# Performance work log

Hardware: AMD Instinct MI355X
Metric: run time of the kernel (lower is better)

The kernel has to match this reference:

```python
import jax, jax.numpy as jnp
import numpy as np

B, L, DIM, H, HD = 1, 2048, 3072, 24, 128
RANK, ALPHA, LORA_WEIGHT = 16, 16.0, 1.0
LORA_SCALE = ALPHA / RANK * LORA_WEIGHT


def _rope_pe(seq_len, head_dim, theta=10000.0):
    # Flux rope: pe[l, d/2, 2, 2] rotation matrices, returned as [1,1,L,d/2,2,2]
    pos = jnp.arange(seq_len, dtype=jnp.float32)
    omega = 1.0 / (theta ** (jnp.arange(0, head_dim, 2, dtype=jnp.float32) / head_dim))
    ang = pos[:, None] * omega[None, :]                      # [L, HD/2]
    cos, sin = jnp.cos(ang), jnp.sin(ang)
    pe = jnp.stack([jnp.stack([cos, -sin], -1),
                    jnp.stack([sin, cos], -1)], -2)          # [L, HD/2, 2, 2]
    return pe[None, None]                                    # [1,1,L,HD/2,2,2]


def setup_inputs() -> dict:
    key = jax.random.key(0)
    ks = jax.random.split(key, 8)
    std = 0.02
    return {
        "x": jax.random.normal(ks[0], (B, L, DIM), jnp.float32),
        "pe": _rope_pe(L, HD),
        "qkv_w": jax.random.normal(ks[1], (3 * DIM, DIM), jnp.float32) * std,
        "qkv_b": jnp.zeros((3 * DIM,), jnp.float32),
        "proj_w": jax.random.normal(ks[2], (DIM, DIM), jnp.float32) * std,
        "proj_b": jnp.zeros((DIM,), jnp.float32),
        # torch init: down ~ N(0, 1/rank); up is zeros at init but we use small randn
        # so the LoRA path is numerically active for kernel testing.
        "qkv_down": jax.random.normal(ks[3], (RANK, DIM), jnp.float32) / RANK,
        "qkv_up": jax.random.normal(ks[4], (3 * DIM, RANK), jnp.float32) * std,
        "proj_down": jax.random.normal(ks[5], (RANK, DIM), jnp.float32) / RANK,
        "proj_up": jax.random.normal(ks[6], (DIM, RANK), jnp.float32) * std,
        "q_scale": jnp.ones((HD,), jnp.float32),
        "k_scale": jnp.ones((HD,), jnp.float32),
    }


def _rmsnorm(t, scale):
    # Flux QKNorm: per-head RMSNorm with learned scale over head_dim
    return t * jax.lax.rsqrt(jnp.mean(t * t, axis=-1, keepdims=True) + 1e-6) * scale


def _apply_rope(t, pe):
    # t: [B,H,L,HD]; pe: [1,1,L,HD/2,2,2]; out[...,i] = pe[...,i,0]*t0 + pe[...,i,1]*t1
    t2 = t.reshape(*t.shape[:-1], HD // 2, 2)
    out = jnp.einsum('...ij,...j->...i', pe, t2)
    return out.reshape(t.shape)


def reference(x, pe, qkv_w, qkv_b, proj_w, proj_b,
              qkv_down, qkv_up, proj_down, proj_up, q_scale, k_scale):
    # fused qkv + LoRA epilogue
    qkv = x @ qkv_w.T + qkv_b + ((x @ qkv_down.T) @ qkv_up.T) * LORA_SCALE
    qkv = qkv.reshape(B, L, 3, H, HD).transpose(2, 0, 3, 1, 4)  # [3,B,H,L,HD]
    q, k, v = qkv[0], qkv[1], qkv[2]
    q = _rmsnorm(q, q_scale)
    k = _rmsnorm(k, k_scale)
    q = _apply_rope(q, pe)
    k = _apply_rope(k, pe)
    scores = jnp.einsum('bhqd,bhkd->bhqk', q, k) / jnp.sqrt(jnp.float32(HD))
    p = jax.nn.softmax(scores, axis=-1)
    o = jnp.einsum('bhqk,bhkd->bhqd', p, v)
    o = o.transpose(0, 2, 1, 3).reshape(B, L, H * HD)           # B L (H D)
    # output proj + LoRA epilogue
    out = o @ proj_w.T + proj_b + ((o @ proj_down.T) @ proj_up.T) * LORA_SCALE
    return out
```

## Files before the change

### kernel.cpp

```cpp
#include <hip/hip_runtime.h>
#include <math.h>

#define L_SEQ 2048
#define DIM   3072
#define NH    24
#define HD    128
#define RANK  16
#define N_QKV 9216
#define KE    3136

typedef __attribute__((ext_vector_type(8))) short bf16x8;
typedef __attribute__((ext_vector_type(4))) float f32x4;
typedef unsigned short u16;
typedef unsigned int u32;

__device__ __forceinline__ u16 f2bf(float f) {
    union { float f; u32 u; } v; v.f = f;
    return (u16)((v.u + 0x7fffu + ((v.u >> 16) & 1u)) >> 16);
}
__device__ __forceinline__ float bf2f(u16 h) {
    union { u32 u; float f; } v; v.u = ((u32)h) << 16; return v.f;
}

#define GLOBAL_TO_LDS16(gp, lp) \
  __builtin_amdgcn_global_load_lds((const __attribute__((address_space(1))) u32*)(gp), \
                                   (__attribute__((address_space(3))) u32*)(lp), 16, 0, 0)

__global__ __launch_bounds__(64) void pack_pe_kernel(
    const float* __restrict__ pe, float2* __restrict__ pe2)
{
    int l = blockIdx.x, i = threadIdx.x;
    int base = l * 256 + i * 4;
    float2 cs; cs.x = pe[base]; cs.y = pe[base + 2];
    pe2[l * 64 + i] = cs;
}

__global__ __launch_bounds__(256) void lora_down_kernel(
    const float* __restrict__ X, const float* __restrict__ W, float* __restrict__ T)
{
    int l = blockIdx.x;
    int r = threadIdx.x >> 4;
    int lane = threadIdx.x & 15;
    const float* xr = X + (size_t)l * DIM;
    const float* wr = W + (size_t)r * DIM;
    float s = 0.f;
    for (int k = lane; k < DIM; k += 16) s = fmaf(xr[k], wr[k], s);
    #pragma unroll
    for (int mm = 8; mm; mm >>= 1) s += __shfl_xor(s, mm);
    if (lane == 0) T[l * RANK + r] = s;
}

__global__ __launch_bounds__(256) void lora_down_bf_kernel(
    const u16* __restrict__ X, const float* __restrict__ W, float* __restrict__ T, int pitch)
{
    int l = blockIdx.x;
    int r = threadIdx.x >> 4;
    int lane = threadIdx.x & 15;
    const u16* xr = X + (size_t)l * pitch;
    const float* wr = W + (size_t)r * DIM;
    float s = 0.f;
    for (int k = lane; k < DIM; k += 16) s = fmaf(bf2f(xr[k]), wr[k], s);
    #pragma unroll
    for (int mm = 8; mm; mm >>= 1) s += __shfl_xor(s, mm);
    if (lane == 0) T[l * RANK + r] = s;
}

__global__ __launch_bounds__(256) void pack_w_kernel(
    const float* __restrict__ W, const float* __restrict__ Up, u16* __restrict__ out)
{
    int row = blockIdx.x;
    const float* wr = W + (size_t)row * DIM;
    u16* orow = out + (size_t)row * KE;
    #pragma unroll
    for (int it = 0; it < 3; it++) {
        int c4 = threadIdx.x + it * 256;
        float4 v = ((const float4*)wr)[c4];
        ushort4 o = {f2bf(v.x), f2bf(v.y), f2bf(v.z), f2bf(v.w)};
        *(ushort4*)(orow + c4 * 4) = o;
    }
    int t = threadIdx.x;
    if (t < RANK) {
        u16 b = f2bf(Up[row * RANK + t]);
        orow[DIM + t] = b;
        orow[DIM + RANK + t] = b;
    } else if (t >= 32 && t < 64) {
        orow[DIM + t] = 0;
    }
}

__global__ __launch_bounds__(256) void pack_x_kernel(
    const float* __restrict__ X, const float* __restrict__ T, u16* __restrict__ out)
{
    int row = blockIdx.x;
    const float* xr = X + (size_t)row * DIM;
    u16* orow = out + (size_t)row * KE;
    #pragma unroll
    for (int it = 0; it < 3; it++) {
        int c4 = threadIdx.x + it * 256;
        float4 v = ((const float4*)xr)[c4];
        ushort4 o = {f2bf(v.x), f2bf(v.y), f2bf(v.z), f2bf(v.w)};
        *(ushort4*)(orow + c4 * 4) = o;
    }
    int t = threadIdx.x;
    if (t < RANK) {
        float tv = T[row * RANK + t];
        u16 hi = f2bf(tv);
        orow[DIM + t] = hi;
        orow[DIM + RANK + t] = f2bf(tv - bf2f(hi));
    } else if (t >= 32 && t < 64) {
        orow[DIM + t] = 0;
    }
}

__global__ __launch_bounds__(64) void pack_t_kernel(
    const float* __restrict__ T, u16* __restrict__ out)
{
    int row = blockIdx.x, t = threadIdx.x;
    u16* orow = out + (size_t)row * KE;
    if (t < RANK) {
        float tv = T[row * RANK + t];
        u16 hi = f2bf(tv);
        orow[DIM + t] = hi;
        orow[DIM + RANK + t] = f2bf(tv - bf2f(hi));
    } else if (t >= 32) {
        orow[DIM + t] = 0;
    }
}

template<int MODE>
__global__ __launch_bounds__(256) void gemm_mfma_kernel(
    const u16* __restrict__ A, const u16* __restrict__ W,
    const float* __restrict__ bias,
    float* __restrict__ Cf,
    u16* __restrict__ qkbf, u16* __restrict__ vT,
    const float2* __restrict__ pe2,
    const float* __restrict__ q_scale, const float* __restrict__ k_scale,
    int M, int N, int K)
{
    __shared__ __align__(16) u16 a_s[2][128 * 64];
    __shared__ __align__(16) u16 b_s[2][128 * 64];

    int tid = threadIdx.x;
    int wave = tid >> 6, lane = tid & 63;
    int quad = lane >> 4, l15 = lane & 15;
    int wm = wave >> 1, wn = wave & 1;

    int num_n = N >> 7;
    int xcd = blockIdx.x & 7;
    int loc = blockIdx.x >> 3;
    int bm = (((xcd & 3) << 2) + (loc & 3)) << 7;
    int bn = ((xcd >> 2) * (num_n >> 1) + (loc >> 2)) << 7;

    const u16* ga[4]; const u16* gb[4];
    u16 *lA[4], *lB[4];
    #pragma unroll
    for (int e = 0; e < 4; e++) {
        int r = e * 32 + (tid >> 3);
        int g = (tid & 7) ^ (r & 7);
        ga[e] = A + (size_t)(bm + r) * K + g * 8;
        gb[e] = W + (size_t)(bn + r) * K + g * 8;
        lA[e] = &a_s[0][(e * 32 + wave * 8) * 64];
        lB[e] = &b_s[0][(e * 32 + wave * 8) * 64];
    }

    f32x4 acc[4][4];
    #pragma unroll
    for (int i = 0; i < 4; i++)
        #pragma unroll
        for (int j = 0; j < 4; j++) acc[i][j] = (f32x4){0.f, 0.f, 0.f, 0.f};

    int abase[4], bbase[4], co[2];
    #pragma unroll
    for (int i = 0; i < 4; i++) {
        abase[i] = (wm * 64 + i * 16 + l15) * 64;
        bbase[i] = (wn * 64 + i * 16 + l15) * 64;
    }
    #pragma unroll
    for (int ks = 0; ks < 2; ks++) co[ks] = ((ks * 4 + quad) ^ (l15 & 7)) * 8;

    #pragma unroll
    for (int e = 0; e < 4; e++) {
        GLOBAL_TO_LDS16(ga[e], lA[e]);
        GLOBAL_TO_LDS16(gb[e], lB[e]);
    }
    asm volatile("s_waitcnt vmcnt(0)" ::: "memory");
    __builtin_amdgcn_s_barrier();

    int nt = K >> 6;
    for (int t = 0; t < nt; ++t) {
        int cur = t & 1;
        int cb = cur * 8192;
        int nb = (cur ^ 1) * 8192;
        if (t + 1 < nt) {
            int ko = (t + 1) << 6;
            #pragma unroll
            for (int e = 0; e < 4; e++) {
                GLOBAL_TO_LDS16(ga[e] + ko, lA[e] + nb);
                GLOBAL_TO_LDS16(gb[e] + ko, lB[e] + nb);
            }
        }
        __builtin_amdgcn_s_setprio(1);
        #pragma unroll
        for (int ks = 0; ks < 2; ks++) {
            bf16x8 af[4], bf[4];
            #pragma unroll
            for (int i = 0; i < 4; i++) af[i] = *(const bf16x8*)&a_s[0][cb + abase[i] + co[ks]];
            #pragma unroll
            for (int j = 0; j < 4; j++) bf[j] = *(const bf16x8*)&b_s[0][cb + bbase[j] + co[ks]];
            #pragma unroll
            for (int i = 0; i < 4; i++)
                #pragma unroll
                for (int j = 0; j < 4; j++)
                    acc[i][j] = __builtin_amdgcn_mfma_f32_16x16x32_bf16(af[i], bf[j], acc[i][j], 0, 0, 0);
        }
        __builtin_amdgcn_s_setprio(0);
        asm volatile("s_waitcnt vmcnt(0)" ::: "memory");
        __builtin_amdgcn_s_barrier();
    }

    if (MODE == 0) {
        #pragma unroll
        for (int j = 0; j < 4; j++) {
            int col = bn + wn * 64 + j * 16 + l15;
            float bj = bias[col];
            #pragma unroll
            for (int i = 0; i < 4; i++)
                #pragma unroll
                for (int r = 0; r < 4; r++) {
                    int row = bm + wm * 64 + i * 16 + quad * 4 + r;
                    Cf[(size_t)row * N + col] = acc[i][j][r] + bj;
                }
        }
        return;
    }

    int tn = bn >> 7;
    int mq = (tn >= 48) ? 2 : (tn >= 24 ? 1 : 0);
    int h = tn - mq * 24;

    #pragma unroll
    for (int j = 0; j < 4; j++) {
        float bj = bias[bn + wn * 64 + j * 16 + l15];
        #pragma unroll
        for (int i = 0; i < 4; i++)
            #pragma unroll
            for (int r = 0; r < 4; r++) acc[i][j][r] += bj;
    }

    if (mq == 2) {
        #pragma unroll
        for (int j = 0; j < 4; j++) {
            int d = wn * 64 + j * 16 + l15;
            u16* vrow = vT + ((size_t)h * HD + d) * L_SEQ;
            #pragma unroll
            for (int i = 0; i < 4; i++)
                #pragma unroll
                for (int r = 0; r < 4; r++) {
                    int kv = bm + wm * 64 + i * 16 + quad * 4 + r;
                    int slot = ((kv >> 3) & 7) ^ (d & 7);
                    int colp = (kv & ~63) + slot * 8 + (kv & 7);
                    vrow[colp] = f2bf(acc[i][j][r]);
                }
        }
    } else {
        float ssp[4][4];
        #pragma unroll
        for (int i = 0; i < 4; i++)
            #pragma unroll
            for (int r = 0; r < 4; r++) {
                float s = 0.f;
                #pragma unroll
                for (int j = 0; j < 4; j++) s = fmaf(acc[i][j][r], acc[i][j][r], s);
                #pragma unroll
                for (int mm = 8; mm; mm >>= 1) s += __shfl_xor(s, mm);
                ssp[i][r] = s;
            }
        float* ss_s = (float*)a_s;
        if (l15 == 0) {
            #pragma unroll
            for (int i = 0; i < 4; i++)
                *(float4*)&ss_s[wn * 128 + wm * 64 + i * 16 + quad * 4] =
                    make_float4(ssp[i][0], ssp[i][1], ssp[i][2], ssp[i][3]);
        }
        __syncthreads();
        float rfac[4][4];
        #pragma unroll
        for (int i = 0; i < 4; i++) {
            float4 s0 = *(const float4*)&ss_s[wm * 64 + i * 16 + quad * 4];
            float4 s1 = *(const float4*)&ss_s[128 + wm * 64 + i * 16 + quad * 4];
            rfac[i][0] = rsqrtf((s0.x + s1.x) * (1.f / HD) + 1e-6f);
            rfac[i][1] = rsqrtf((s0.y + s1.y) * (1.f / HD) + 1e-6f);
            rfac[i][2] = rsqrtf((s0.z + s1.z) * (1.f / HD) + 1e-6f);
            rfac[i][3] = rsqrtf((s0.w + s1.w) * (1.f / HD) + 1e-6f);
        }
        const float* scale = mq ? k_scale : q_scale;
        float sgn = (l15 & 1) ? 1.f : -1.f;
        u16* obase = qkbf + (size_t)(mq * NH + h) * L_SEQ * HD;
        #pragma unroll
        for (int j = 0; j < 4; j++) {
            int d = wn * 64 + j * 16 + l15;
            float sd = scale[d];
            #pragma unroll
            for (int i = 0; i < 4; i++)
                #pragma unroll
                for (int r = 0; r < 4; r++) {
                    int row = bm + wm * 64 + i * 16 + quad * 4 + r;
                    float t = acc[i][j][r] * rfac[i][r] * sd;
                    float tp = __shfl_xor(t, 1);
                    float2 cs = pe2[row * 64 + (d >> 1)];
                    float o = fmaf(cs.x, t, sgn * cs.y * tp);
                    obase[(size_t)row * HD + d] = f2bf(o);
                }
        }
    }
}

__global__ __launch_bounds__(256) void attn_mfma_kernel(
    const u16* __restrict__ qk_bf, const u16* __restrict__ vT, u16* __restrict__ Og)
{
    __shared__ __align__(16) u16 k_s[64 * 128];
    __shared__ __align__(16) u16 v_s[128 * 64];
    __shared__ __align__(16) u16 p_s[4][16 * 72];

    int bid = blockIdx.x;
    int loc = bid >> 3;
    int h = (bid & 7) * 3 + (loc >> 5);
    int q0 = (loc & 31) * 64;
    int tid = threadIdx.x;
    int wave = tid >> 6, lane = tid & 63;
    int quad = lane >> 4, l15 = lane & 15;
    const u16* qb = qk_bf + (size_t)h * L_SEQ * HD;
    const u16* kb = qk_bf + (size_t)(NH + h) * L_SEQ * HD;
    const u16* vTh = vT + (size_t)h * HD * L_SEQ;

    bf16x8 aq[4];
    {
        const u16* qr = qb + (size_t)(q0 + wave * 16 + l15) * HD + quad * 8;
        #pragma unroll
        for (int ks = 0; ks < 4; ks++) aq[ks] = *(const bf16x8*)(qr + ks * 32);
    }

    f32x4 o_acc[8];
    #pragma unroll
    for (int n = 0; n < 8; n++) o_acc[n] = (f32x4){0.f, 0.f, 0.f, 0.f};
    float lsum[4] = {0.f, 0.f, 0.f, 0.f};
    const float sc = 0.08838834764831845f * 1.4426950408889634f;
    const float MB = 64.0f;

    const u16* gk[4];
    #pragma unroll
    for (int e = 0; e < 4; e++) {
        int r = wave * 16 + e * 4 + (lane >> 4);
        int g = l15 ^ (r & 15);
        gk[e] = kb + (size_t)r * HD + g * 8;
    }
    const u16* gv[4];
    #pragma unroll
    for (int e = 0; e < 4; e++) {
        int d = wave * 32 + e * 8 + (lane >> 3);
        gv[e] = vTh + (size_t)d * L_SEQ + (lane & 7) * 8;
    }
    int vco[2];
    #pragma unroll
    for (int ks = 0; ks < 2; ks++) vco[ks] = ((ks * 4 + quad) ^ (l15 & 7)) * 8;

    for (int kv0 = 0; kv0 < L_SEQ; kv0 += 64) {
        __syncthreads();
        #pragma unroll
        for (int e = 0; e < 4; e++) {
            GLOBAL_TO_LDS16(gk[e] + (size_t)kv0 * HD, &k_s[(wave * 16 + e * 4) * 128]);
            GLOBAL_TO_LDS16(gv[e] + kv0, &v_s[(wave * 32 + e * 8) * 64]);
        }
        __syncthreads();

        f32x4 sacc[4];
        #pragma unroll
        for (int j = 0; j < 4; j++) sacc[j] = (f32x4){0.f, 0.f, 0.f, 0.f};
        #pragma unroll
        for (int ks = 0; ks < 4; ks++) {
            #pragma unroll
            for (int j = 0; j < 4; j++) {
                int n = j * 16 + l15;
                int slot = (ks * 4 + quad) ^ (n & 15);
                bf16x8 bk = *(const bf16x8*)&k_s[n * 128 + slot * 8];
                sacc[j] = __builtin_amdgcn_mfma_f32_16x16x32_bf16(aq[ks], bk, sacc[j], 0, 0, 0);
            }
        }

        #pragma unroll
        for (int j = 0; j < 4; j++)
            #pragma unroll
            for (int r = 0; r < 4; r++) {
                float p = exp2f(fmaf(sacc[j][r], sc, -MB));
                sacc[j][r] = p;
                lsum[r] += p;
                p_s[wave][(quad * 4 + r) * 72 + j * 16 + l15] = f2bf(p);
            }
        bf16x8 ap[2];
        #pragma unroll
        for (int ks = 0; ks < 2; ks++)
            ap[ks] = *(const bf16x8*)&p_s[wave][l15 * 72 + ks * 32 + quad * 8];

        #pragma unroll
        for (int ks = 0; ks < 2; ks++) {
            #pragma unroll
            for (int n = 0; n < 8; n++) {
                bf16x8 bv = *(const bf16x8*)&v_s[(n * 16 + l15) * 64 + vco[ks]];
                o_acc[n] = __builtin_amdgcn_mfma_f32_16x16x32_bf16(ap[ks], bv, o_acc[n], 0, 0, 0);
            }
        }
    }

    #pragma unroll
    for (int r = 0; r < 4; r++) {
        #pragma unroll
        for (int mm = 8; mm; mm >>= 1) lsum[r] += __shfl_xor(lsum[r], mm);
    }

    #pragma unroll
    for (int r = 0; r < 4; r++) {
        float inv = 1.f / lsum[r];
        int row = q0 + wave * 16 + quad * 4 + r;
        u16* orow = Og + (size_t)row * KE + h * HD;
        #pragma unroll
        for (int n = 0; n < 8; n++)
            orow[n * 16 + l15] = f2bf(o_acc[n][r] * inv);
    }
}

extern "C" void kernel_launch(void* const* d_in, const int* in_sizes, int n_in,
                              void* d_out, int out_size, void* d_ws, size_t ws_size,
                              hipStream_t stream)
{
    const float* x         = (const float*)d_in[0];
    const float* pe        = (const float*)d_in[1];
    const float* qkv_w     = (const float*)d_in[2];
    const float* qkv_b     = (const float*)d_in[3];
    const float* proj_w    = (const float*)d_in[4];
    const float* proj_b    = (const float*)d_in[5];
    const float* qkv_down  = (const float*)d_in[6];
    const float* qkv_up    = (const float*)d_in[7];
    const float* proj_down = (const float*)d_in[8];
    const float* proj_up   = (const float*)d_in[9];
    const float* q_scale   = (const float*)d_in[10];
    const float* k_scale   = (const float*)d_in[11];
    float* out = (float*)d_out;

    char* w = (char*)d_ws;
    u16*   qk_bf  = (u16*)w;    w += (size_t)2 * NH * L_SEQ * HD * 2;
    u16*   vT_bf  = (u16*)w;    w += (size_t)NH * HD * L_SEQ * 2;
    u16*   x_ext  = (u16*)w;    w += (size_t)L_SEQ * KE * 2;
    u16*   wq_ext = (u16*)w;    w += (size_t)N_QKV * KE * 2;
    u16*   wp_ext = (u16*)w;    w += (size_t)DIM * KE * 2;
    u16*   o_ext  = (u16*)w;    w += (size_t)L_SEQ * KE * 2;
    float2* pe2   = (float2*)w; w += (size_t)L_SEQ * 64 * sizeof(float2);
    float* t1     = (float*)w;  w += (size_t)L_SEQ * RANK * 4;
    float* t2     = (float*)w;

    pack_pe_kernel<<<L_SEQ, 64, 0, stream>>>(pe, pe2);
    pack_w_kernel<<<N_QKV, 256, 0, stream>>>(qkv_w, qkv_up, wq_ext);
    pack_w_kernel<<<DIM, 256, 0, stream>>>(proj_w, proj_up, wp_ext);
    lora_down_kernel<<<L_SEQ, 256, 0, stream>>>(x, qkv_down, t1);
    pack_x_kernel<<<L_SEQ, 256, 0, stream>>>(x, t1, x_ext);

    gemm_mfma_kernel<1><<<(N_QKV / 128) * (L_SEQ / 128), 256, 0, stream>>>(
        x_ext, wq_ext, qkv_b, nullptr, qk_bf, vT_bf, pe2, q_scale, k_scale,
        L_SEQ, N_QKV, KE);
    attn_mfma_kernel<<<(L_SEQ / 64) * NH, 256, 0, stream>>>(qk_bf, vT_bf, o_ext);
    lora_down_bf_kernel<<<L_SEQ, 256, 0, stream>>>(o_ext, proj_down, t2, KE);
    pack_t_kernel<<<L_SEQ, 64, 0, stream>>>(t2, o_ext);
    gemm_mfma_kernel<0><<<(DIM / 128) * (L_SEQ / 128), 256, 0, stream>>>(
        o_ext, wp_ext, proj_b, out, nullptr, nullptr, nullptr, nullptr, nullptr,
        L_SEQ, DIM, KE);
}
```

Measured before the change: 689.4 us.

## Enlarge GEMM tiles to 256x256 with 512-thread blocks

Both MFMA GEMMs move from 128x128 tiles with 4 waves to 256x256 tiles with 8 waves, each wave computing a 128x64 sub-tile. The aim is to roughly halve global and LDS loads per MFMA through more operand reuse. The block-to-tile mapping becomes a linear XCD-strided swizzle. The fused QKV epilogue is reworked so each tile spans two heads: RMSNorm row sums are paired across wave columns and the head index comes from the wave column. In exchange the grid shrinks to 288 and 96 blocks and each block needs 128KB of LDS, which risks poor CU fill and wave quantization, especially for the projection GEMM.

```diff
diff --git a/kernel.cpp b/kernel.cpp
--- a/kernel.cpp
+++ b/kernel.cpp
@@ -128,7 +128,7 @@
 }
 
 template<int MODE>
-__global__ __launch_bounds__(256) void gemm_mfma_kernel(
+__global__ __launch_bounds__(512) void gemm_mfma_kernel(
     const u16* __restrict__ A, const u16* __restrict__ W,
     const float* __restrict__ bias,
     float* __restrict__ Cf,
@@ -137,44 +137,42 @@
     const float* __restrict__ q_scale, const float* __restrict__ k_scale,
     int M, int N, int K)
 {
-    __shared__ __align__(16) u16 a_s[2][128 * 64];
-    __shared__ __align__(16) u16 b_s[2][128 * 64];
+    __shared__ __align__(16) u16 a_s[2][256 * 64];
+    __shared__ __align__(16) u16 b_s[2][256 * 64];
 
     int tid = threadIdx.x;
     int wave = tid >> 6, lane = tid & 63;
     int quad = lane >> 4, l15 = lane & 15;
-    int wm = wave >> 1, wn = wave & 1;
-
-    int num_n = N >> 7;
-    int xcd = blockIdx.x & 7;
-    int loc = blockIdx.x >> 3;
-    int bm = (((xcd & 3) << 2) + (loc & 3)) << 7;
-    int bn = ((xcd >> 2) * (num_n >> 1) + (loc >> 2)) << 7;
+    int wm = wave >> 2, wn = wave & 3;
+
+    int num_m = M >> 8, num_n = N >> 8;
+    int swz = (blockIdx.x & 7) * ((num_m * num_n) >> 3) + (blockIdx.x >> 3);
+    int bm = (swz % num_m) << 8;
+    int bn = (swz / num_m) << 8;
 
     const u16* ga[4]; const u16* gb[4];
     u16 *lA[4], *lB[4];
     #pragma unroll
     for (int e = 0; e < 4; e++) {
-        int r = e * 32 + (tid >> 3);
+        int r = e * 64 + (tid >> 3);
         int g = (tid & 7) ^ (r & 7);
         ga[e] = A + (size_t)(bm + r) * K + g * 8;
         gb[e] = W + (size_t)(bn + r) * K + g * 8;
-        lA[e] = &a_s[0][(e * 32 + wave * 8) * 64];
-        lB[e] = &b_s[0][(e * 32 + wave * 8) * 64];
-    }
-
-    f32x4 acc[4][4];
-    #pragma unroll
-    for (int i = 0; i < 4; i++)
+        lA[e] = &a_s[0][(e * 64 + wave * 8) * 64];
+        lB[e] = &b_s[0][(e * 64 + wave * 8) * 64];
+    }
+
+    f32x4 acc[8][4];
+    #pragma unroll
+    for (int i = 0; i < 8; i++)
         #pragma unroll
         for (int j = 0; j < 4; j++) acc[i][j] = (f32x4){0.f, 0.f, 0.f, 0.f};
 
-    int abase[4], bbase[4], co[2];
-    #pragma unroll
-    for (int i = 0; i < 4; i++) {
-        abase[i] = (wm * 64 + i * 16 + l15) * 64;
-        bbase[i] = (wn * 64 + i * 16 + l15) * 64;
-    }
+    int abase[8], bbase[4], co[2];
+    #pragma unroll
+    for (int i = 0; i < 8; i++) abase[i] = (wm * 128 + i * 16 + l15) * 64;
+    #pragma unroll
+    for (int j = 0; j < 4; j++) bbase[j] = (wn * 64 + j * 16 + l15) * 64;
     #pragma unroll
     for (int ks = 0; ks < 2; ks++) co[ks] = ((ks * 4 + quad) ^ (l15 & 7)) * 8;
 
@@ -189,8 +187,8 @@
     int nt = K >> 6;
     for (int t = 0; t < nt; ++t) {
         int cur = t & 1;
-        int cb = cur * 8192;
-        int nb = (cur ^ 1) * 8192;
+        int cb = cur * 16384;
+        int nb = (cur ^ 1) * 16384;
         if (t + 1 < nt) {
             int ko = (t + 1) << 6;
             #pragma unroll
@@ -202,13 +200,13 @@
         __builtin_amdgcn_s_setprio(1);
         #pragma unroll
         for (int ks = 0; ks < 2; ks++) {
-            bf16x8 af[4], bf[4];
-            #pragma unroll
-            for (int i = 0; i < 4; i++) af[i] = *(const bf16x8*)&a_s[0][cb + abase[i] + co[ks]];
+            bf16x8 af[8], bf[4];
+            #pragma unroll
+            for (int i = 0; i < 8; i++) af[i] = *(const bf16x8*)&a_s[0][cb + abase[i] + co[ks]];
             #pragma unroll
             for (int j = 0; j < 4; j++) bf[j] = *(const bf16x8*)&b_s[0][cb + bbase[j] + co[ks]];
             #pragma unroll
-            for (int i = 0; i < 4; i++)
+            for (int i = 0; i < 8; i++)
                 #pragma unroll
                 for (int j = 0; j < 4; j++)
                     acc[i][j] = __builtin_amdgcn_mfma_f32_16x16x32_bf16(af[i], bf[j], acc[i][j], 0, 0, 0);
@@ -224,25 +222,26 @@
             int col = bn + wn * 64 + j * 16 + l15;
             float bj = bias[col];
             #pragma unroll
-            for (int i = 0; i < 4; i++)
+            for (int i = 0; i < 8; i++)
                 #pragma unroll
                 for (int r = 0; r < 4; r++) {
-                    int row = bm + wm * 64 + i * 16 + quad * 4 + r;
+                    int row = bm + wm * 128 + i * 16 + quad * 4 + r;
                     Cf[(size_t)row * N + col] = acc[i][j][r] + bj;
                 }
         }
         return;
     }
 
-    int tn = bn >> 7;
-    int mq = (tn >= 48) ? 2 : (tn >= 24 ? 1 : 0);
-    int h = tn - mq * 24;
+    int mq = (bn >= 2 * DIM) ? 2 : (bn >= DIM ? 1 : 0);
+    int h0 = (bn - mq * DIM) >> 7;
+    int h = h0 + (wn >> 1);
+    int d = (wn & 1) * 64;
 
     #pragma unroll
     for (int j = 0; j < 4; j++) {
         float bj = bias[bn + wn * 64 + j * 16 + l15];
         #pragma unroll
-        for (int i = 0; i < 4; i++)
+        for (int i = 0; i < 8; i++)
             #pragma unroll
             for (int r = 0; r < 4; r++) acc[i][j][r] += bj;
     }
@@ -250,22 +249,22 @@
     if (mq == 2) {
         #pragma unroll
         for (int j = 0; j < 4; j++) {
-            int d = wn * 64 + j * 16 + l15;
-            u16* vrow = vT + ((size_t)h * HD + d) * L_SEQ;
-            #pragma unroll
-            for (int i = 0; i < 4; i++)
+            int dd = d + j * 16 + l15;
+            u16* vrow = vT + ((size_t)h * HD + dd) * L_SEQ;
+            #pragma unroll
+            for (int i = 0; i < 8; i++)
                 #pragma unroll
                 for (int r = 0; r < 4; r++) {
-                    int kv = bm + wm * 64 + i * 16 + quad * 4 + r;
-                    int slot = ((kv >> 3) & 7) ^ (d & 7);
+                    int kv = bm + wm * 128 + i * 16 + quad * 4 + r;
+                    int slot = ((kv >> 3) & 7) ^ (dd & 7);
                     int colp = (kv & ~63) + slot * 8 + (kv & 7);
                     vrow[colp] = f2bf(acc[i][j][r]);
                 }
         }
     } else {
-        float ssp[4][4];
-        #pragma unroll
-        for (int i = 0; i < 4; i++)
+        float ssp[8][4];
+        #pragma unroll
+        for (int i = 0; i < 8; i++)
             #pragma unroll
             for (int r = 0; r < 4; r++) {
                 float s = 0.f;
@@ -278,16 +277,17 @@
         float* ss_s = (float*)a_s;
         if (l15 == 0) {
             #pragma unroll
-            for (int i = 0; i < 4; i++)
-                *(float4*)&ss_s[wn * 128 + wm * 64 + i * 16 + quad * 4] =
+            for (int i = 0; i < 8; i++)
+                *(float4*)&ss_s[wn * 256 + wm * 128 + i * 16 + quad * 4] =
                     make_float4(ssp[i][0], ssp[i][1], ssp[i][2], ssp[i][3]);
         }
         __syncthreads();
-        float rfac[4][4];
-        #pragma unroll
-        for (int i = 0; i < 4; i++) {
-            float4 s0 = *(const float4*)&ss_s[wm * 64 + i * 16 + quad * 4];
-            float4 s1 = *(const float4*)&ss_s[128 + wm * 64 + i * 16 + quad * 4];
+        float rfac[8][4];
+        #pragma unroll
+        for (int i = 0; i < 8; i++) {
+            int base = wm * 128 + i * 16 + quad * 4;
+            float4 s0 = *(const float4*)&ss_s[(wn & ~1) * 256 + base];
+            float4 s1 = *(const float4*)&ss_s[(wn | 1) * 256 + base];
             rfac[i][0] = rsqrtf((s0.x + s1.x) * (1.f / HD) + 1e-6f);
             rfac[i][1] = rsqrtf((s0.y + s1.y) * (1.f / HD) + 1e-6f);
             rfac[i][2] = rsqrtf((s0.z + s1.z) * (1.f / HD) + 1e-6f);
@@ -298,18 +298,18 @@
         u16* obase = qkbf + (size_t)(mq * NH + h) * L_SEQ * HD;
         #pragma unroll
         for (int j = 0; j < 4; j++) {
-            int d = wn * 64 + j * 16 + l15;
-            float sd = scale[d];
-            #pragma unroll
-            for (int i = 0; i < 4; i++)
+            int dd = d + j * 16 + l15;
+            float sd = scale[dd];
+            #pragma unroll
+            for (int i = 0; i < 8; i++)
                 #pragma unroll
                 for (int r = 0; r < 4; r++) {
-                    int row = bm + wm * 64 + i * 16 + quad * 4 + r;
+                    int row = bm + wm * 128 + i * 16 + quad * 4 + r;
                     float t = acc[i][j][r] * rfac[i][r] * sd;
                     float tp = __shfl_xor(t, 1);
-                    float2 cs = pe2[row * 64 + (d >> 1)];
+                    float2 cs = pe2[row * 64 + (dd >> 1)];
                     float o = fmaf(cs.x, t, sgn * cs.y * tp);
-                    obase[(size_t)row * HD + d] = f2bf(o);
+                    obase[(size_t)row * HD + dd] = f2bf(o);
                 }
         }
     }
@@ -463,13 +463,13 @@
     lora_down_kernel<<<L_SEQ, 256, 0, stream>>>(x, qkv_down, t1);
     pack_x_kernel<<<L_SEQ, 256, 0, stream>>>(x, t1, x_ext);
 
-    gemm_mfma_kernel<1><<<(N_QKV / 128) * (L_SEQ / 128), 256, 0, stream>>>(
+    gemm_mfma_kernel<1><<<(N_QKV / 256) * (L_SEQ / 256), 512, 0, stream>>>(
         x_ext, wq_ext, qkv_b, nullptr, qk_bf, vT_bf, pe2, q_scale, k_scale,
         L_SEQ, N_QKV, KE);
     attn_mfma_kernel<<<(L_SEQ / 64) * NH, 256, 0, stream>>>(qk_bf, vT_bf, o_ext);
     lora_down_bf_kernel<<<L_SEQ, 256, 0, stream>>>(o_ext, proj_down, t2, KE);
     pack_t_kernel<<<L_SEQ, 64, 0, stream>>>(t2, o_ext);
-    gemm_mfma_kernel<0><<<(DIM / 128) * (L_SEQ / 128), 256, 0, stream>>>(
+    gemm_mfma_kernel<0><<<(DIM / 256) * (L_SEQ / 256), 512, 0, stream>>>(
         o_ext, wp_ext, proj_b, out, nullptr, nullptr, nullptr, nullptr, nullptr,
         L_SEQ, DIM, KE);
 }
```

Result: slower. 833.9 us (+21.0%).

## Double-buffer K/V tiles in attention and use partial vmcnt waits in GEMM

Applied to the files above, without the earlier changes.

The attention kernel gets two LDS buffers for K and V, so the next tile's global-to-LDS load is issued before computing on the current one. The old loop loaded synchronously each iteration. In both the GEMM and attention loops the full vmcnt(0) wait becomes vmcnt(8), which waits only for the current tile's loads while the prefetch stays in flight. s_setprio is also added around the attention MFMA sections. Doubling K/V LDS use raises the attention kernel's shared memory by about 32KB, which may cut occupancy.

```diff
diff --git a/kernel.cpp b/kernel.cpp
--- a/kernel.cpp
+++ b/kernel.cpp
@@ -183,8 +183,6 @@
         GLOBAL_TO_LDS16(ga[e], lA[e]);
         GLOBAL_TO_LDS16(gb[e], lB[e]);
     }
-    asm volatile("s_waitcnt vmcnt(0)" ::: "memory");
-    __builtin_amdgcn_s_barrier();
 
     int nt = K >> 6;
     for (int t = 0; t < nt; ++t) {
@@ -198,7 +196,11 @@
                 GLOBAL_TO_LDS16(ga[e] + ko, lA[e] + nb);
                 GLOBAL_TO_LDS16(gb[e] + ko, lB[e] + nb);
             }
-        }
+            asm volatile("s_waitcnt vmcnt(8)" ::: "memory");
+        } else {
+            asm volatile("s_waitcnt vmcnt(0)" ::: "memory");
+        }
+        __builtin_amdgcn_s_barrier();
         __builtin_amdgcn_s_setprio(1);
         #pragma unroll
         for (int ks = 0; ks < 2; ks++) {
@@ -214,7 +216,6 @@
                     acc[i][j] = __builtin_amdgcn_mfma_f32_16x16x32_bf16(af[i], bf[j], acc[i][j], 0, 0, 0);
         }
         __builtin_amdgcn_s_setprio(0);
-        asm volatile("s_waitcnt vmcnt(0)" ::: "memory");
         __builtin_amdgcn_s_barrier();
     }
 
@@ -318,8 +319,8 @@
 __global__ __launch_bounds__(256) void attn_mfma_kernel(
     const u16* __restrict__ qk_bf, const u16* __restrict__ vT, u16* __restrict__ Og)
 {
-    __shared__ __align__(16) u16 k_s[64 * 128];
-    __shared__ __align__(16) u16 v_s[128 * 64];
+    __shared__ __align__(16) u16 k_s[2][64 * 128];
+    __shared__ __align__(16) u16 v_s[2][128 * 64];
     __shared__ __align__(16) u16 p_s[4][16 * 72];
 
     int bid = blockIdx.x;
@@ -348,44 +349,67 @@
     const float MB = 64.0f;
 
     const u16* gk[4];
+    u16* lK[4];
     #pragma unroll
     for (int e = 0; e < 4; e++) {
         int r = wave * 16 + e * 4 + (lane >> 4);
         int g = l15 ^ (r & 15);
         gk[e] = kb + (size_t)r * HD + g * 8;
+        lK[e] = &k_s[0][(wave * 16 + e * 4) * 128];
     }
     const u16* gv[4];
+    u16* lV[4];
     #pragma unroll
     for (int e = 0; e < 4; e++) {
         int d = wave * 32 + e * 8 + (lane >> 3);
         gv[e] = vTh + (size_t)d * L_SEQ + (lane & 7) * 8;
+        lV[e] = &v_s[0][(wave * 32 + e * 8) * 64];
     }
     int vco[2];
     #pragma unroll
     for (int ks = 0; ks < 2; ks++) vco[ks] = ((ks * 4 + quad) ^ (l15 & 7)) * 8;
 
-    for (int kv0 = 0; kv0 < L_SEQ; kv0 += 64) {
-        __syncthreads();
-        #pragma unroll
-        for (int e = 0; e < 4; e++) {
-            GLOBAL_TO_LDS16(gk[e] + (size_t)kv0 * HD, &k_s[(wave * 16 + e * 4) * 128]);
-            GLOBAL_TO_LDS16(gv[e] + kv0, &v_s[(wave * 32 + e * 8) * 64]);
-        }
-        __syncthreads();
+    #pragma unroll
+    for (int e = 0; e < 4; e++) {
+        GLOBAL_TO_LDS16(gk[e], lK[e]);
+        GLOBAL_TO_LDS16(gv[e], lV[e]);
+    }
+
+    const int NT = L_SEQ / 64;
+    for (int t = 0; t < NT; ++t) {
+        int cur = t & 1;
+        int kcb = cur * (64 * 128);
+        int vcb = cur * (128 * 64);
+        if (t + 1 < NT) {
+            int kv1 = (t + 1) * 64;
+            int nk = (cur ^ 1) * (64 * 128);
+            int nv = (cur ^ 1) * (128 * 64);
+            #pragma unroll
+            for (int e = 0; e < 4; e++) {
+                GLOBAL_TO_LDS16(gk[e] + (size_t)kv1 * HD, lK[e] + nk);
+                GLOBAL_TO_LDS16(gv[e] + kv1, lV[e] + nv);
+            }
+            asm volatile("s_waitcnt vmcnt(8)" ::: "memory");
+        } else {
+            asm volatile("s_waitcnt vmcnt(0)" ::: "memory");
+        }
+        __builtin_amdgcn_s_barrier();
 
         f32x4 sacc[4];
         #pragma unroll
         for (int j = 0; j < 4; j++) sacc[j] = (f32x4){0.f, 0.f, 0.f, 0.f};
+        __builtin_amdgcn_s_setprio(1);
         #pragma unroll
         for (int ks = 0; ks < 4; ks++) {
             #pragma unroll
             for (int j = 0; j < 4; j++) {
                 int n = j * 16 + l15;
                 int slot = (ks * 4 + quad) ^ (n & 15);
-                bf16x8 bk = *(const bf16x8*)&k_s[n * 128 + slot * 8];
+                bf16x8 bk = *(const bf16x8*)&k_s[0][kcb + n * 128 + slot * 8];
                 sacc[j] = __builtin_amdgcn_mfma_f32_16x16x32_bf16(aq[ks], bk, sacc[j], 0, 0, 0);
             }
         }
+        __builtin_amdgcn_s_setprio(0);
 
         #pragma unroll
         for (int j = 0; j < 4; j++)
@@ -401,14 +425,17 @@
         for (int ks = 0; ks < 2; ks++)
             ap[ks] = *(const bf16x8*)&p_s[wave][l15 * 72 + ks * 32 + quad * 8];
 
+        __builtin_amdgcn_s_setprio(1);
         #pragma unroll
         for (int ks = 0; ks < 2; ks++) {
             #pragma unroll
             for (int n = 0; n < 8; n++) {
-                bf16x8 bv = *(const bf16x8*)&v_s[(n * 16 + l15) * 64 + vco[ks]];
+                bf16x8 bv = *(const bf16x8*)&v_s[0][vcb + (n * 16 + l15) * 64 + vco[ks]];
                 o_acc[n] = __builtin_amdgcn_mfma_f32_16x16x32_bf16(ap[ks], bv, o_acc[n], 0, 0, 0);
             }
         }
+        __builtin_amdgcn_s_setprio(0);
+        __builtin_amdgcn_s_barrier();
     }
 
     #pragma unroll
```

Result: slower. 713.7 us (+3.5%).
